# Kernel tuning notes

Hardware: AMD Instinct MI355X
Metric: run time of the kernel (lower is better)

Reference implementation:

```python
import jax, jax.numpy as jnp
import numpy as np

N = 100000      # entities
E = 400000      # triples (KG1)
EH = 400000     # half of symmetric all-edge list
R = 2000        # relations (rel1_size)
RH = 100        # r_hidden
EHID = 300      # e_hidden
LGE = 60000     # line-graph edges
NEG_SLOPE = 0.01


def seg_softmax(e, idx, num):
    # PyG-style segment softmax with max-subtraction and +1e-16 denom
    m = jax.ops.segment_max(e, idx, num_segments=num)
    p = jnp.exp(e - m[idx])
    s = jax.ops.segment_sum(p, idx, num_segments=num)
    return p / (s[idx] + 1e-16)


def gcn(x, w, ei):
    j, i = ei[0], ei[1]
    deg = jax.ops.segment_sum(jnp.ones(ei.shape[1], x.dtype), i, num_segments=x.shape[0])
    dinv = jnp.where(deg > 0, deg ** -0.5, 0.0)
    norm = dinv[j] * dinv[i]                       # [E]
    xw = x @ w.T                                   # [N,300]
    out = jax.ops.segment_sum(norm[:, None] * xw[j], i, num_segments=x.shape[0])
    return jax.nn.relu(out)


def highway(x1, x2, w, b):
    g = jax.nn.sigmoid(x1 @ w.T + b)
    return g * x2 + (1.0 - g) * x1


def l_gat(x, ei, val):
    j, i = ei[0], ei[1]
    n = x.shape[0]
    vi = seg_softmax(val, i, n)
    vj = seg_softmax(val, j, n)
    alpha = seg_softmax(vi + vj, j, n)
    return jax.nn.relu(jax.ops.segment_sum(alpha[:, None] * x[j], i, num_segments=n))


def gat(x, r_emb, ei, rel_e, a_i, a_j, a_r):
    j, i = ei[0], ei[1]
    e = (x @ a_i)[i] + (x @ a_j)[j] + (r_emb @ a_r)[rel_e]
    alpha = seg_softmax(jax.nn.leaky_relu(e, NEG_SLOPE), i, x.shape[0])
    return jax.nn.relu(jax.ops.segment_sum(alpha[:, None] * x[j], i, num_segments=x.shape[0]))


def gat_r_to_e(x_e, x_r, ei, rel_e, a_h, a_t, a_r):
    h, t = ei[0], ei[1]
    n_e = x_e.shape[0]
    eh = (x_e @ a_h)[h]
    et = (x_e @ a_t)[t]
    er = (x_r @ a_r)[rel_e]
    a1 = seg_softmax(jax.nn.leaky_relu(eh + er, NEG_SLOPE), h, n_e)
    x_h = jax.ops.segment_sum(a1[:, None] * x_r[rel_e], h, num_segments=n_e)
    a2 = seg_softmax(jax.nn.leaky_relu(et + er, NEG_SLOPE), t, n_e)
    x_t = jax.ops.segment_sum(a2[:, None] * x_r[rel_e], t, num_segments=n_e)
    return jnp.concatenate([x_h, x_t], axis=1)


def setup_inputs() -> dict:
    key = jax.random.key(0)
    ks = jax.random.split(key, 24)
    # symmetric all-edge graph (guarantees nonzero degrees at touched nodes)
    src = jax.random.randint(ks[0], (EH,), 0, N, dtype=jnp.int32)
    dst = jax.random.randint(ks[1], (EH,), 0, N, dtype=jnp.int32)
    edge_index_all = jnp.stack([jnp.concatenate([src, dst]), jnp.concatenate([dst, src])])
    rel_all = jax.random.randint(ks[2], (2 * EH,), 0, 2 * R, dtype=jnp.int32)
    edge_index = jnp.stack([jax.random.randint(ks[3], (E,), 0, N, dtype=jnp.int32),
                            jax.random.randint(ks[4], (E,), 0, N, dtype=jnp.int32)])
    rel = jax.random.randint(ks[5], (E,), 0, R, dtype=jnp.int32)
    lg_merge = jax.random.randint(ks[6], (2, LGE), 0, R, dtype=jnp.int32)
    lg_triangular = jax.random.randint(ks[7], (2, LGE), 0, R, dtype=jnp.int32)
    merge_val = jax.random.normal(ks[8], (LGE,), jnp.float32)
    tri_val = jax.random.normal(ks[9], (LGE,), jnp.float32)
    x_e = jax.random.normal(ks[10], (N, EHID), jnp.float32)
    s = 0.05
    return {
        'x_e': x_e, 'merge_val': merge_val, 'tri_val': tri_val,
        'gcn1_w': s * jax.random.normal(ks[11], (EHID, EHID), jnp.float32),
        'hw1_w': s * jax.random.normal(ks[12], (EHID, EHID), jnp.float32),
        'hw1_b': jnp.zeros((EHID,), jnp.float32),
        'gcn2_w': s * jax.random.normal(ks[13], (EHID, EHID), jnp.float32),
        'hw2_w': s * jax.random.normal(ks[14], (EHID, EHID), jnp.float32),
        'hw2_b': jnp.zeros((EHID,), jnp.float32),
        'rel_emb_out1': s * jax.random.normal(ks[15], (R, RH), jnp.float32),
        'rel_emb_tri1': s * jax.random.normal(ks[16], (R, RH), jnp.float32),
        'hwr_w': s * jax.random.normal(ks[17], (RH, RH), jnp.float32),
        'hwr_b': jnp.zeros((RH,), jnp.float32),
        'gat_ai': s * jax.random.normal(ks[18], (EHID,), jnp.float32),
        'gat_aj': s * jax.random.normal(ks[19], (EHID,), jnp.float32),
        'gat_ar': s * jax.random.normal(ks[20], (2 * RH,), jnp.float32),
        'g2e_ah': s * jax.random.normal(ks[21], (2 * EHID,), jnp.float32),
        'g2e_at': s * jax.random.normal(ks[22], (2 * EHID,), jnp.float32),
        'g2e_ar': s * jax.random.normal(ks[23], (RH,), jnp.float32),
        'edge_index': edge_index, 'rel': rel,
        'edge_index_all': edge_index_all, 'rel_all': rel_all,
        'lg_merge': lg_merge, 'lg_triangular': lg_triangular,
    }


def reference(x_e, merge_val, tri_val, gcn1_w, hw1_w, hw1_b, gcn2_w, hw2_w, hw2_b,
              rel_emb_out1, rel_emb_tri1, hwr_w, hwr_b, gat_ai, gat_aj, gat_ar,
              g2e_ah, g2e_at, g2e_ar, edge_index, rel, edge_index_all, rel_all,
              lg_merge, lg_triangular):
    x = highway(x_e, gcn(x_e, gcn1_w, edge_index_all), hw1_w, hw1_b)
    x = highway(x, gcn(x, gcn2_w, edge_index_all), hw2_w, hw2_b)
    # rel.max()+1 == rel1_size branch (KG1)
    rel_merge = l_gat(rel_emb_out1, lg_merge, merge_val)      # [R,RH]
    rel_tri = l_gat(rel_emb_tri1, lg_triangular, tri_val)     # [R,RH]
    x_r = highway(rel_merge, rel_tri, hwr_w, hwr_b)           # [R,RH]
    rel_cat = jnp.concatenate([rel_merge, rel_tri], axis=1)   # [R,2RH]
    rel_emb = jnp.concatenate([rel_cat, rel_cat], axis=0)     # [2R,2RH]
    x = jnp.concatenate([x, gat(x, rel_emb, edge_index_all, rel_all, gat_ai, gat_aj, gat_ar)], axis=1)  # [N,600]
    x = jnp.concatenate([x, gat_r_to_e(x, x_r, edge_index, rel, g2e_ah, g2e_at, g2e_ar)], axis=1)        # [N,800]
    return x
```

## Files before the change

kernel.cpp:

```cpp
#include <hip/hip_runtime.h>

#define WAVE 64
#define CDIV(a,b) (((a)+(b)-1)/(b))
#define XBS 320

typedef float f32x16 __attribute__((ext_vector_type(16)));
typedef unsigned short u16x8 __attribute__((ext_vector_type(8)));

__device__ __forceinline__ unsigned short f2bf_rne(float f) {
    unsigned u = __float_as_uint(f);
    unsigned r = (u + 0x7FFFu + ((u >> 16) & 1u)) >> 16;
    return (unsigned short)r;
}
__device__ __forceinline__ float bf2f(unsigned short h) {
    return __uint_as_float(((unsigned)h) << 16);
}
__device__ __forceinline__ float2 bfp2f(ushort2 u) {
    float2 r; r.x = bf2f(u.x); r.y = bf2f(u.y); return r;
}
__device__ __forceinline__ float sigm(float x) { return 1.0f / (1.0f + expf(-x)); }

#define MFMA32(acc, a, b) \
    asm volatile("v_mfma_f32_32x32x16_bf16 %0, %1, %2, %0" : "+v"(acc) : "v"(a), "v"(b))

__device__ __forceinline__ unsigned f2mono(float f) {
    unsigned u = __float_as_uint(f);
    return (u & 0x80000000u) ? ~u : (u | 0x80000000u);
}
__device__ __forceinline__ float mono2f(unsigned u) {
    return (u & 0x80000000u) ? __uint_as_float(u & 0x7fffffffu) : __uint_as_float(~u);
}
__device__ __forceinline__ float leaky(float v) { return (v > 0.0f) ? v : 0.01f*v; }

__device__ __forceinline__ long fragoff(long r, int k, int npk) {
    return ((r >> 5) * (long)npk + (k >> 4)) * 512
         + (((k >> 3) & 1) << 8) + ((r & 31) << 3) + (k & 7);
}

__global__ void k_cvt_pack1(const float* __restrict__ src, long ld, int rows, int K, int npk,
                            int roff, unsigned short* __restrict__ dst)
{
    int nc4 = npk << 2;
    long idx = (long)blockIdx.x*blockDim.x + threadIdx.x;
    if (idx >= (long)rows * nc4) return;
    long r = idx / nc4; int k = (int)(idx % nc4) << 2;
    float4 v = {0.0f, 0.0f, 0.0f, 0.0f};
    if (k + 4 <= K) v = *(const float4*)(src + r*ld + k);
    ushort4 h;
    h.x = f2bf_rne(v.x); h.y = f2bf_rne(v.y); h.z = f2bf_rne(v.z); h.w = f2bf_rne(v.w);
    *(ushort4*)(dst + fragoff(r + roff, k, npk)) = h;
}

__global__ void k_cvt_w4(const float* __restrict__ g1w, const float* __restrict__ h1w,
                         const float* __restrict__ g2w, const float* __restrict__ h2w,
                         int npk, unsigned short* __restrict__ W0,
                         unsigned short* __restrict__ W1)
{
    const int nc4 = npk << 2;
    const long per = (long)300 * nc4;
    long idx = (long)blockIdx.x*blockDim.x + threadIdx.x;
    if (idx >= 4*per) return;
    int which = (int)(idx / per);
    long lidx = idx % per;
    long r = lidx / nc4; int k = (int)(lidx % nc4) << 2;
    const float* src = (which == 0) ? g1w : (which == 1) ? h1w : (which == 2) ? g2w : h2w;
    unsigned short* dst = (which < 2) ? W0 : W1;
    int roff = (which & 1) ? 320 : 0;
    float4 v = {0.0f, 0.0f, 0.0f, 0.0f};
    if (k + 4 <= 300) v = *(const float4*)(src + r*300 + k);
    ushort4 h;
    h.x = f2bf_rne(v.x); h.y = f2bf_rne(v.y); h.z = f2bf_rne(v.z); h.w = f2bf_rne(v.w);
    *(ushort4*)(dst + fragoff(r + roff, k, npk)) = h;
}

__global__ __launch_bounds__(256, 3)
void k_gemm_frag(const unsigned short* __restrict__ Ab,
                 const unsigned short* __restrict__ Bb,
                 unsigned short* __restrict__ C, long ldc, int M, int N, int nk, int nrb)
{
    const int lane = threadIdx.x & 63;
    const int wid  = threadIdx.x >> 6;
    const int lin  = blockIdx.x;
    const int xcd  = lin & 7;
    const int m    = lin >> 3;
    const int col0 = (m % 5) * 128;
    const int rb   = xcd + ((m / 5) << 3);
    if (rb >= nrb) return;
    const int row0 = rb * 128 + wid * 32;

    const long cs = (long)nk * 512;
    const unsigned short* pA = Ab + (long)(row0 >> 5) * cs + lane * 8;
    const unsigned short* pB = Bb + (long)(col0 >> 5) * cs + lane * 8;

    f32x16 acc[4];
    #pragma unroll
    for (int c = 0; c < 4; ++c) acc[c] = (f32x16)0.0f;

    u16x8 pa, pb0, pb1, pb2, pb3;
    u16x8 qa, qb0, qb1, qb2, qb3;

    #define LOADP(t_) { long o = (long)(t_)*512;                                   \
        pa  = *(const u16x8*)(pA + o);                                             \
        pb0 = *(const u16x8*)(pB + o);        pb1 = *(const u16x8*)(pB + cs + o);  \
        pb2 = *(const u16x8*)(pB + 2*cs + o); pb3 = *(const u16x8*)(pB + 3*cs + o); }
    #define LOADQ(t_) { long o = (long)(t_)*512;                                   \
        qa  = *(const u16x8*)(pA + o);                                             \
        qb0 = *(const u16x8*)(pB + o);        qb1 = *(const u16x8*)(pB + cs + o);  \
        qb2 = *(const u16x8*)(pB + 2*cs + o); qb3 = *(const u16x8*)(pB + 3*cs + o); }
    #define STEPP {                                                                 \
        MFMA32(acc[0], pa, pb0); MFMA32(acc[1], pa, pb1);                           \
        MFMA32(acc[2], pa, pb2); MFMA32(acc[3], pa, pb3); }
    #define STEPQ {                                                                 \
        MFMA32(acc[0], qa, qb0); MFMA32(acc[1], qa, qb1);                           \
        MFMA32(acc[2], qa, qb2); MFMA32(acc[3], qa, qb3); }

    LOADP(0);
    int t = 0;
    for (;;) {
        bool m1 = (t + 1 < nk);
        if (m1) LOADQ(t + 1);
        STEPP;
        if (!m1) break;
        bool m2 = (t + 2 < nk);
        if (m2) LOADP(t + 2);
        STEPQ;
        if (!m2) break;
        t += 2;
    }
    #undef LOADP
    #undef LOADQ
    #undef STEPP
    #undef STEPQ

    const int crow0 = row0 + 4*(lane >> 5);
    const int ccol0 = col0 + (lane & 31);
    #pragma unroll
    for (int c = 0; c < 4; ++c) {
        int col = ccol0 + c*32;
        if (col >= N) continue;
        #pragma unroll
        for (int reg = 0; reg < 16; ++reg) {
            int row = crow0 + (reg & 3) + 8*(reg >> 2);
            if (row < M) C[(long)row*ldc + col] = f2bf_rne(acc[c][reg]);
        }
    }
}

#define GBM 64
#define GBN 64
#define GBK 16
__global__ __launch_bounds__(256)
void k_gemm(const float* __restrict__ A, long lda,
            const float* __restrict__ B, long ldb,
            float* __restrict__ C, long ldc,
            int M, int N, int K)
{
    __shared__ float As[GBK][GBM + 4];
    __shared__ float Bs[GBK][GBN + 4];
    const int tid = threadIdx.x;
    const int tx = tid & 15, ty = tid >> 4;
    const int row0 = blockIdx.y * GBM, col0 = blockIdx.x * GBN;
    float acc[4][4] = {};
    for (int kt = 0; kt < K; kt += GBK) {
        #pragma unroll
        for (int p = 0; p < 4; ++p) {
            int mn = (tid >> 4) + p * 16;
            int k  = tid & 15;
            int gk = kt + k;
            int gr = row0 + mn;
            As[k][mn] = (gr < M && gk < K) ? A[(long)gr * lda + gk] : 0.0f;
            int gc = col0 + mn;
            Bs[k][mn] = (gc < N && gk < K) ? B[(long)gc * ldb + gk] : 0.0f;
        }
        __syncthreads();
        #pragma unroll
        for (int kk = 0; kk < GBK; ++kk) {
            float a0 = As[kk][ty*4+0], a1 = As[kk][ty*4+1];
            float a2 = As[kk][ty*4+2], a3 = As[kk][ty*4+3];
            float b0 = Bs[kk][tx*4+0], b1 = Bs[kk][tx*4+1];
            float b2 = Bs[kk][tx*4+2], b3 = Bs[kk][tx*4+3];
            acc[0][0] += a0*b0; acc[0][1] += a0*b1; acc[0][2] += a0*b2; acc[0][3] += a0*b3;
            acc[1][0] += a1*b0; acc[1][1] += a1*b1; acc[1][2] += a1*b2; acc[1][3] += a1*b3;
            acc[2][0] += a2*b0; acc[2][1] += a2*b1; acc[2][2] += a2*b2; acc[2][3] += a2*b3;
            acc[3][0] += a3*b0; acc[3][1] += a3*b1; acc[3][2] += a3*b2; acc[3][3] += a3*b3;
        }
        __syncthreads();
    }
    #pragma unroll
    for (int i2 = 0; i2 < 4; ++i2)
        #pragma unroll
        for (int j2 = 0; j2 < 4; ++j2) {
            int r = row0 + ty*4 + i2, c = col0 + tx*4 + j2;
            if (r < M && c < N) C[(long)r*ldc + c] = acc[i2][j2];
        }
}

__global__ void k_hist3(const int* __restrict__ iA, const int* __restrict__ hE,
                        const int* __restrict__ tE, int* __restrict__ cnt,
                        int EA, int E, int N) {
    int e = blockIdx.x*blockDim.x + threadIdx.x;
    int tot = EA + 2*E;
    if (e >= tot) return;
    if (e < EA)            atomicAdd(&cnt[iA[e]], 1);
    else if (e < EA + E)   atomicAdd(&cnt[N + hE[e - EA]], 1);
    else                   atomicAdd(&cnt[2*N + tE[e - EA - E]], 1);
}
__global__ void k_scan1(const int* __restrict__ in, int* __restrict__ out,
                        int* __restrict__ bsum, int n) {
    __shared__ int sh[512];
    int gid = blockIdx.x*512 + threadIdx.x;
    int v = (gid < n) ? in[gid] : 0;
    sh[threadIdx.x] = v; __syncthreads();
    for (int o = 1; o < 512; o <<= 1) {
        int t = (threadIdx.x >= o) ? sh[threadIdx.x - o] : 0;
        __syncthreads();
        sh[threadIdx.x] += t;
        __syncthreads();
    }
    if (gid < n) out[gid] = sh[threadIdx.x] - v;
    if (threadIdx.x == 511) bsum[blockIdx.x] = sh[511];
}
__global__ void k_scan2(int* __restrict__ bsum, int nb) {
    __shared__ int sh[1024];
    int v = (threadIdx.x < nb) ? bsum[threadIdx.x] : 0;
    sh[threadIdx.x] = v; __syncthreads();
    for (int o = 1; o < 1024; o <<= 1) {
        int t = (threadIdx.x >= o) ? sh[threadIdx.x - o] : 0;
        __syncthreads();
        sh[threadIdx.x] += t;
        __syncthreads();
    }
    if (threadIdx.x < nb) bsum[threadIdx.x] = sh[threadIdx.x] - v;
}
__global__ void k_scan3(int* __restrict__ out, const int* __restrict__ bsum, int n) {
    int gid = blockIdx.x*512 + threadIdx.x;
    if (gid < n) out[gid] += bsum[blockIdx.x];
}
__global__ void k_fill3(const int* __restrict__ iA, const int* __restrict__ hE,
                        const int* __restrict__ tE, const int* __restrict__ rowptr,
                        int* __restrict__ cursor, int* __restrict__ perm,
                        int EA, int E, int N) {
    int e = blockIdx.x*blockDim.x + threadIdx.x;
    int tot = EA + 2*E;
    if (e >= tot) return;
    int key, le;
    if (e < EA)          { le = e;          key = iA[le]; }
    else if (e < EA + E) { le = e - EA;     key = N + hE[le]; }
    else                 { le = e - EA - E; key = 2*N + tE[le]; }
    int p = rowptr[key] + atomicAdd(&cursor[key], 1);
    perm[p] = le;
}
__global__ void k_dinv_cnt(const int* __restrict__ cnt, float* __restrict__ dinv, int n) {
    int i = blockIdx.x*blockDim.x + threadIdx.x;
    if (i < n) { int c = cnt[i]; dinv[i] = (c > 0) ? rsqrtf((float)c) : 0.0f; }
}
__global__ void k_prep_gcn(const int* __restrict__ perm, const int* __restrict__ jA,
                           const int* __restrict__ iA, const float* __restrict__ dinv,
                           int* __restrict__ jp, float* __restrict__ nm, int E) {
    int p = blockIdx.x*blockDim.x + threadIdx.x;
    if (p >= E) return;
    int e = perm[p];
    int j = jA[e];
    jp[p] = j;
    nm[p] = dinv[iA[e]] * dinv[j];
}
__global__ void k_permute3(const int* __restrict__ rel_all, const int* __restrict__ rel,
                           const int* __restrict__ perm, int* __restrict__ relp,
                           int EA, int E, int R) {
    int p = blockIdx.x*blockDim.x + threadIdx.x;
    int tot = EA + 2*E;
    if (p >= tot) return;
    if (p < EA) relp[p] = rel_all[perm[p]] % R;
    else        relp[p] = rel[perm[p]];
}

__global__ void k_gather_hw(const unsigned short* __restrict__ xg, long ldx,
                            const unsigned short* __restrict__ gl,
                            const float* __restrict__ x1f,
                            const unsigned short* __restrict__ x1b,
                            const float* __restrict__ bias,
                            const int* __restrict__ jp, const float* __restrict__ nm,
                            const int* __restrict__ rowptr, const int* __restrict__ cnt,
                            float* __restrict__ outp, long ldo,
                            unsigned short* __restrict__ pk,
                            unsigned short* __restrict__ xbf,
                            const float* __restrict__ ai, const float* __restrict__ aj,
                            float* __restrict__ sa, float* __restrict__ sb,
                            int npk, int n)
{
    int w = (blockIdx.x*blockDim.x + threadIdx.x) >> 6;
    int lane = threadIdx.x & 63;
    if (w >= n) return;
    int beg = rowptr[w], end = beg + cnt[w];
    const int i0 = lane, i1 = lane + 64, i2 = lane + 128;
    const bool t3 = (lane < 22);
    float2 a0 = {0,0}, a1 = {0,0}, a2 = {0,0};
    int e = beg;
    for (; e + 8 <= end; e += 8) {
        long jj[8]; float wt[8];
        #pragma unroll
        for (int u = 0; u < 8; ++u) { jj[u] = jp[e+u]; wt[u] = nm[e+u]; }
        #pragma unroll
        for (int u = 0; u < 8; ++u) {
            float2 v = bfp2f(((const ushort2*)(xg + jj[u]*ldx))[i0]);
            a0.x += wt[u]*v.x; a0.y += wt[u]*v.y;
        }
        #pragma unroll
        for (int u = 0; u < 8; ++u) {
            float2 v = bfp2f(((const ushort2*)(xg + jj[u]*ldx))[i1]);
            a1.x += wt[u]*v.x; a1.y += wt[u]*v.y;
        }
        if (t3) {
            #pragma unroll
            for (int u = 0; u < 8; ++u) {
                float2 v = bfp2f(((const ushort2*)(xg + jj[u]*ldx))[i2]);
                a2.x += wt[u]*v.x; a2.y += wt[u]*v.y;
            }
        }
    }
    for (; e + 4 <= end; e += 4) {
        long jj[4]; float wt[4];
        #pragma unroll
        for (int u = 0; u < 4; ++u) { jj[u] = jp[e+u]; wt[u] = nm[e+u]; }
        #pragma unroll
        for (int u = 0; u < 4; ++u) {
            float2 v = bfp2f(((const ushort2*)(xg + jj[u]*ldx))[i0]);
            a0.x += wt[u]*v.x; a0.y += wt[u]*v.y;
        }
        #pragma unroll
        for (int u = 0; u < 4; ++u) {
            float2 v = bfp2f(((const ushort2*)(xg + jj[u]*ldx))[i1]);
            a1.x += wt[u]*v.x; a1.y += wt[u]*v.y;
        }
        if (t3) {
            #pragma unroll
            for (int u = 0; u < 4; ++u) {
                float2 v = bfp2f(((const ushort2*)(xg + jj[u]*ldx))[i2]);
                a2.x += wt[u]*v.x; a2.y += wt[u]*v.y;
            }
        }
    }
    for (; e < end; ++e) {
        long j0 = jp[e]; float w0 = nm[e];
        float2 v;
        v = bfp2f(((const ushort2*)(xg + j0*ldx))[i0]); a0.x += w0*v.x; a0.y += w0*v.y;
        v = bfp2f(((const ushort2*)(xg + j0*ldx))[i1]); a1.x += w0*v.x; a1.y += w0*v.y;
        if (t3) { v = bfp2f(((const ushort2*)(xg + j0*ldx))[i2]); a2.x += w0*v.x; a2.y += w0*v.y; }
    }
    const ushort2* glr = (const ushort2*)(gl + (long)w*ldx);
    const float2*  x1r = (const float2*)(x1f + (long)w*300);
    const ushort2* x1r2 = (const ushort2*)(x1b + (long)w*XBS);
    const float2*  br  = (const float2*)bias;
    float2 o0 = {0,0}, o1 = {0,0}, o2 = {0,0};
    {
        float2 gv = bfp2f(glr[i0]); float2 bv = br[i0];
        float2 xv = x1f ? x1r[i0] : bfp2f(x1r2[i0]);
        float g0 = sigm(gv.x + bv.x), g1 = sigm(gv.y + bv.y);
        o0.x = g0*fmaxf(a0.x,0.0f) + (1.0f-g0)*xv.x;
        o0.y = g1*fmaxf(a0.y,0.0f) + (1.0f-g1)*xv.y;
    }
    {
        float2 gv = bfp2f(glr[i1]); float2 bv = br[i1];
        float2 xv = x1f ? x1r[i1] : bfp2f(x1r2[i1]);
        float g0 = sigm(gv.x + bv.x), g1 = sigm(gv.y + bv.y);
        o1.x = g0*fmaxf(a1.x,0.0f) + (1.0f-g0)*xv.x;
        o1.y = g1*fmaxf(a1.y,0.0f) + (1.0f-g1)*xv.y;
    }
    if (t3) {
        float2 gv = bfp2f(glr[i2]); float2 bv = br[i2];
        float2 xv = x1f ? x1r[i2] : bfp2f(x1r2[i2]);
        float g0 = sigm(gv.x + bv.x), g1 = sigm(gv.y + bv.y);
        o2.x = g0*fmaxf(a2.x,0.0f) + (1.0f-g0)*xv.x;
        o2.y = g1*fmaxf(a2.y,0.0f) + (1.0f-g1)*xv.y;
    }
    if (outp) {
        float2* dst = (float2*)(outp + (long)w*ldo);
        dst[i0] = o0; dst[i1] = o1;
        if (t3) dst[i2] = o2;
    }
    if (pk) {
        auto pack2 = [&](int k, float2 o) {
            ushort2 hv; hv.x = f2bf_rne(o.x); hv.y = f2bf_rne(o.y);
            *(ushort2*)(pk + fragoff(w, k, npk)) = hv;
        };
        pack2(2*lane, o0);
        pack2(128 + 2*lane, o1);
        if (t3) pack2(256 + 2*lane, o2);
        else if (lane < 24) {
            ushort2 z = {0,0};
            *(ushort2*)(pk + fragoff(w, 256 + 2*lane, npk)) = z;
        }
    }
    if (xbf) {
        ushort2* xw = (ushort2*)(xbf + (long)w*XBS);
        ushort2 t;
        t.x = f2bf_rne(o0.x); t.y = f2bf_rne(o0.y); xw[i0] = t;
        t.x = f2bf_rne(o1.x); t.y = f2bf_rne(o1.y); xw[i1] = t;
        if (t3) { t.x = f2bf_rne(o2.x); t.y = f2bf_rne(o2.y); xw[i2] = t; }
    }
    if (sa) {
        const float2* ai2 = (const float2*)ai;
        const float2* aj2 = (const float2*)aj;
        float2 A0 = ai2[i0], A1 = ai2[i1], J0 = aj2[i0], J1 = aj2[i1];
        float sva = o0.x*A0.x + o0.y*A0.y + o1.x*A1.x + o1.y*A1.y;
        float svb = o0.x*J0.x + o0.y*J0.y + o1.x*J1.x + o1.y*J1.y;
        if (t3) {
            float2 A2 = ai2[i2], J2 = aj2[i2];
            sva += o2.x*A2.x + o2.y*A2.y;
            svb += o2.x*J2.x + o2.y*J2.y;
        }
        #pragma unroll
        for (int o = 32; o > 0; o >>= 1) {
            sva += __shfl_down(sva, o);
            svb += __shfl_down(svb, o);
        }
        if (lane == 0) { sa[w] = sva; sb[w] = svb; }
    }
}

__global__ void k_gat300(const unsigned short* __restrict__ xbf,
                         const float* __restrict__ sA, const float* __restrict__ sB,
                         const float* __restrict__ rsc,
                         const int* __restrict__ jp, const int* __restrict__ relp,
                         const int* __restrict__ rowptr, const int* __restrict__ cnt,
                         float* __restrict__ out, long ldo,
                         const float* __restrict__ ah, const float* __restrict__ at,
                         float* __restrict__ sh, float* __restrict__ st,
                         int n)
{
    int w = (blockIdx.x*blockDim.x + threadIdx.x) >> 6;
    int lane = threadIdx.x & 63;
    if (w >= n) return;
    int beg = rowptr[w], c = cnt[w];
    const int i0 = lane, i1 = lane + 64, i2 = lane + 128;
    const bool t3 = (lane < 22);
    float2 a0 = {0,0}, a1 = {0,0}, a2 = {0,0};
    if (c > 0) {
        float base = sA[w];
        int   jc = 0;
        float sval = -3.4e38f;
        if (lane < c) {
            jc = jp[beg + lane];
            sval = leaky(base + sB[jc] + rsc[relp[beg + lane]]);
        }
        float mx = sval;
        for (int t = 64 + lane; t < c; t += 64)
            mx = fmaxf(mx, leaky(base + sB[jp[beg+t]] + rsc[relp[beg+t]]));
        #pragma unroll
        for (int o = 32; o > 0; o >>= 1) mx = fmaxf(mx, __shfl_xor(mx, o));
        float pexp = (lane < c) ? expf(sval - mx) : 0.0f;
        float ss = pexp;
        for (int t = 64 + lane; t < c; t += 64)
            ss += expf(leaky(base + sB[jp[beg+t]] + rsc[relp[beg+t]]) - mx);
        #pragma unroll
        for (int o = 32; o > 0; o >>= 1) ss += __shfl_xor(ss, o);
        float inv = 1.0f / (ss + 1e-16f);
        int q = 0;
        int cc = (c < 64) ? c : 64;
        for (; q + 8 <= cc; q += 8) {
            float al[8]; long jj[8];
            #pragma unroll
            for (int u = 0; u < 8; ++u) {
                al[u] = __shfl(pexp, q+u) * inv;
                jj[u] = __shfl(jc, q+u);
            }
            #pragma unroll
            for (int u = 0; u < 8; ++u) {
                float2 v = bfp2f(((const ushort2*)(xbf + jj[u]*XBS))[i0]);
                a0.x += al[u]*v.x; a0.y += al[u]*v.y;
            }
            #pragma unroll
            for (int u = 0; u < 8; ++u) {
                float2 v = bfp2f(((const ushort2*)(xbf + jj[u]*XBS))[i1]);
                a1.x += al[u]*v.x; a1.y += al[u]*v.y;
            }
            if (t3) {
                #pragma unroll
                for (int u = 0; u < 8; ++u) {
                    float2 v = bfp2f(((const ushort2*)(xbf + jj[u]*XBS))[i2]);
                    a2.x += al[u]*v.x; a2.y += al[u]*v.y;
                }
            }
        }
        for (; q + 4 <= cc; q += 4) {
            float al[4]; long jj[4];
            #pragma unroll
            for (int u = 0; u < 4; ++u) {
                al[u] = __shfl(pexp, q+u) * inv;
                jj[u] = __shfl(jc, q+u);
            }
            #pragma unroll
            for (int u = 0; u < 4; ++u) {
                float2 v = bfp2f(((const ushort2*)(xbf + jj[u]*XBS))[i0]);
                a0.x += al[u]*v.x; a0.y += al[u]*v.y;
            }
            #pragma unroll
            for (int u = 0; u < 4; ++u) {
                float2 v = bfp2f(((const ushort2*)(xbf + jj[u]*XBS))[i1]);
                a1.x += al[u]*v.x; a1.y += al[u]*v.y;
            }
            if (t3) {
                #pragma unroll
                for (int u = 0; u < 4; ++u) {
                    float2 v = bfp2f(((const ushort2*)(xbf + jj[u]*XBS))[i2]);
                    a2.x += al[u]*v.x; a2.y += al[u]*v.y;
                }
            }
        }
        for (; q < c; ++q) {
            float al; long j0;
            if (q < 64) { al = __shfl(pexp, q) * inv; j0 = __shfl(jc, q); }
            else {
                j0 = jp[beg + q];
                al = expf(leaky(base + sB[(int)j0] + rsc[relp[beg+q]]) - mx) * inv;
            }
            float2 v;
            v = bfp2f(((const ushort2*)(xbf + j0*XBS))[i0]); a0.x += al*v.x; a0.y += al*v.y;
            v = bfp2f(((const ushort2*)(xbf + j0*XBS))[i1]); a1.x += al*v.x; a1.y += al*v.y;
            if (t3) { v = bfp2f(((const ushort2*)(xbf + j0*XBS))[i2]); a2.x += al*v.x; a2.y += al*v.y; }
        }
    }
    a0.x = fmaxf(a0.x, 0.0f); a0.y = fmaxf(a0.y, 0.0f);
    a1.x = fmaxf(a1.x, 0.0f); a1.y = fmaxf(a1.y, 0.0f);
    a2.x = fmaxf(a2.x, 0.0f); a2.y = fmaxf(a2.y, 0.0f);
    float2* dst = (float2*)(out + (long)w*ldo);
    dst[i0] = a0; dst[i1] = a1;
    if (t3) dst[i2] = a2;
    {
        const ushort2* xw = (const ushort2*)(xbf + (long)w*XBS);
        const float2* ahL = (const float2*)ah;
        const float2* atL = (const float2*)at;
        const float2* ahH = (const float2*)(ah + 300);
        const float2* atH = (const float2*)(at + 300);
        float2 x0 = bfp2f(xw[i0]), x1v = bfp2f(xw[i1]);
        float svh = x0.x*ahL[i0].x + x0.y*ahL[i0].y + x1v.x*ahL[i1].x + x1v.y*ahL[i1].y
                  + a0.x*ahH[i0].x + a0.y*ahH[i0].y + a1.x*ahH[i1].x + a1.y*ahH[i1].y;
        float svt = x0.x*atL[i0].x + x0.y*atL[i0].y + x1v.x*atL[i1].x + x1v.y*atL[i1].y
                  + a0.x*atH[i0].x + a0.y*atH[i0].y + a1.x*atH[i1].x + a1.y*atH[i1].y;
        if (t3) {
            float2 x2v = bfp2f(xw[i2]);
            svh += x2v.x*ahL[i2].x + x2v.y*ahL[i2].y + a2.x*ahH[i2].x + a2.y*ahH[i2].y;
            svt += x2v.x*atL[i2].x + x2v.y*atL[i2].y + a2.x*atH[i2].x + a2.y*atH[i2].y;
        }
        #pragma unroll
        for (int o = 32; o > 0; o >>= 1) {
            svh += __shfl_down(svh, o);
            svt += __shfl_down(svt, o);
        }
        if (lane == 0) { sh[w] = svh; st[w] = svt; }
    }
}

__global__ void k_gather_rel2(const float* __restrict__ xr,
                              const float* __restrict__ sH, const float* __restrict__ sT,
                              const float* __restrict__ srel,
                              const int* __restrict__ relp,
                              const int* __restrict__ rowptrH, const int* __restrict__ cntH,
                              const int* __restrict__ rowptrT, const int* __restrict__ cntT,
                              float* __restrict__ out, long ldo, int n)
{
    int gw = (blockIdx.x*blockDim.x + threadIdx.x) >> 6;
    int lane = threadIdx.x & 63;
    if (gw >= 2*n) return;
    const bool isT = (gw >= n);
    const int w = isT ? gw - n : gw;
    const float* snode = isT ? sT : sH;
    const int* rowptr = isT ? rowptrT : rowptrH;
    const int* cnt    = isT ? cntT    : cntH;
    float* dst = out + (isT ? 700 : 600) + (long)w*ldo;
    int beg = rowptr[w], c = cnt[w];
    const bool t0 = (lane < 50);
    float2 a0 = {0,0};
    if (c > 0) {
        float base = snode[w];
        int   rc = 0;
        float sval = -3.4e38f;
        if (lane < c) {
            rc = relp[beg + lane];
            sval = leaky(base + srel[rc]);
        }
        float mx = sval;
        for (int t = 64 + lane; t < c; t += 64)
            mx = fmaxf(mx, leaky(base + srel[relp[beg+t]]));
        #pragma unroll
        for (int o = 32; o > 0; o >>= 1) mx = fmaxf(mx, __shfl_xor(mx, o));
        float pexp = (lane < c) ? expf(sval - mx) : 0.0f;
        float ss = pexp;
        for (int t = 64 + lane; t < c; t += 64)
            ss += expf(leaky(base + srel[relp[beg+t]]) - mx);
        #pragma unroll
        for (int o = 32; o > 0; o >>= 1) ss += __shfl_xor(ss, o);
        float inv = 1.0f / (ss + 1e-16f);
        int q = 0;
        int cc = (c < 64) ? c : 64;
        for (; q + 4 <= cc; q += 4) {
            float al0 = __shfl(pexp, q)   * inv;
            float al1 = __shfl(pexp, q+1) * inv;
            float al2 = __shfl(pexp, q+2) * inv;
            float al3 = __shfl(pexp, q+3) * inv;
            long r0i = __shfl(rc, q), r1i = __shfl(rc, q+1);
            long r2i = __shfl(rc, q+2), r3i = __shfl(rc, q+3);
            if (t0) {
                float2 v;
                v = ((const float2*)(xr + r0i*100))[lane]; a0.x += al0*v.x; a0.y += al0*v.y;
                v = ((const float2*)(xr + r1i*100))[lane]; a0.x += al1*v.x; a0.y += al1*v.y;
                v = ((const float2*)(xr + r2i*100))[lane]; a0.x += al2*v.x; a0.y += al2*v.y;
                v = ((const float2*)(xr + r3i*100))[lane]; a0.x += al3*v.x; a0.y += al3*v.y;
            }
        }
        for (; q < c; ++q) {
            float al; long r0i;
            if (q < 64) { al = __shfl(pexp, q) * inv; r0i = __shfl(rc, q); }
            else {
                r0i = relp[beg + q];
                al = expf(leaky(base + srel[(int)r0i]) - mx) * inv;
            }
            if (t0) {
                float2 v = ((const float2*)(xr + r0i*100))[lane];
                a0.x += al*v.x; a0.y += al*v.y;
            }
        }
    }
    if (t0) ((float2*)dst)[lane] = a0;
}

__global__ void k_lgat_max(const float* __restrict__ mval, const float* __restrict__ tval,
                           const int* __restrict__ iM, const int* __restrict__ jM,
                           const int* __restrict__ iT, const int* __restrict__ jT,
                           unsigned* __restrict__ mi, unsigned* __restrict__ mj,
                           int LGE, int R)
{
    int e = blockIdx.x*blockDim.x + threadIdx.x;
    if (e >= 2*LGE) return;
    bool g1 = e >= LGE; int le = g1 ? e - LGE : e;
    float v = g1 ? tval[le] : mval[le];
    int i = (g1 ? iT[le] : iM[le]) + (g1 ? R : 0);
    int j = (g1 ? jT[le] : jM[le]) + (g1 ? R : 0);
    unsigned mv = f2mono(v);
    atomicMax(&mi[i], mv);
    atomicMax(&mj[j], mv);
}
__global__ void k_lgat_sum(const float* __restrict__ mval, const float* __restrict__ tval,
                           const int* __restrict__ iM, const int* __restrict__ jM,
                           const int* __restrict__ iT, const int* __restrict__ jT,
                           const unsigned* __restrict__ mi, const unsigned* __restrict__ mj,
                           float* __restrict__ si, float* __restrict__ sj,
                           int LGE, int R)
{
    int e = blockIdx.x*blockDim.x + threadIdx.x;
    if (e >= 2*LGE) return;
    bool g1 = e >= LGE; int le = g1 ? e - LGE : e;
    float v = g1 ? tval[le] : mval[le];
    int i = (g1 ? iT[le] : iM[le]) + (g1 ? R : 0);
    int j = (g1 ? jT[le] : jM[le]) + (g1 ? R : 0);
    atomicAdd(&si[i], expf(v - mono2f(mi[i])));
    atomicAdd(&sj[j], expf(v - mono2f(mj[j])));
}
__global__ void k_lgat_vsum2(const float* __restrict__ mval, const float* __restrict__ tval,
                             const int* __restrict__ iM, const int* __restrict__ jM,
                             const int* __restrict__ iT, const int* __restrict__ jT,
                             const unsigned* __restrict__ mi, const float* __restrict__ si,
                             const unsigned* __restrict__ mj, const float* __restrict__ sj,
                             float* __restrict__ vsum, int LGE, int R)
{
    int e = blockIdx.x*blockDim.x + threadIdx.x;
    if (e >= 2*LGE) return;
    bool g1 = e >= LGE; int le = g1 ? e - LGE : e;
    float v = g1 ? tval[le] : mval[le];
    int i = (g1 ? iT[le] : iM[le]) + (g1 ? R : 0);
    int j = (g1 ? jT[le] : jM[le]) + (g1 ? R : 0);
    float pi = expf(v - mono2f(mi[i])) / (si[i] + 1e-16f);
    float pj = expf(v - mono2f(mj[j])) / (sj[j] + 1e-16f);
    vsum[e] = pi + pj;
}
__global__ void k_lgat_max2(const float* __restrict__ vsum,
                            const int* __restrict__ jM, const int* __restrict__ jT,
                            unsigned* __restrict__ m2, int LGE, int R)
{
    int e = blockIdx.x*blockDim.x + threadIdx.x;
    if (e >= 2*LGE) return;
    bool g1 = e >= LGE; int le = g1 ? e - LGE : e;
    int j = (g1 ? jT[le] : jM[le]) + (g1 ? R : 0);
    atomicMax(&m2[j], f2mono(vsum[e]));
}
__global__ void k_lgat_sum2(const float* __restrict__ vsum,
                            const int* __restrict__ jM, const int* __restrict__ jT,
                            const unsigned* __restrict__ m2, float* __restrict__ s2,
                            int LGE, int R)
{
    int e = blockIdx.x*blockDim.x + threadIdx.x;
    if (e >= 2*LGE) return;
    bool g1 = e >= LGE; int le = g1 ? e - LGE : e;
    int j = (g1 ? jT[le] : jM[le]) + (g1 ? R : 0);
    atomicAdd(&s2[j], expf(vsum[e] - mono2f(m2[j])));
}
__global__ void k_lgat_agg(const float* __restrict__ vsum,
                           const unsigned* __restrict__ m2, const float* __restrict__ s2,
                           const int* __restrict__ iM, const int* __restrict__ jM,
                           const int* __restrict__ iT, const int* __restrict__ jT,
                           const float* __restrict__ remb1, const float* __restrict__ remb2,
                           float* __restrict__ obuf, int LGE, int R, int RH)
{
    int w = (blockIdx.x*blockDim.x + threadIdx.x) >> 6;
    int lane = threadIdx.x & 63;
    if (w >= 2*LGE) return;
    bool g1 = w >= LGE; int le = g1 ? w - LGE : w;
    int o = g1 ? R : 0;
    int i = (g1 ? iT[le] : iM[le]) + o;
    int j = (g1 ? jT[le] : jM[le]);
    float alpha = expf(vsum[w] - mono2f(m2[o + j])) / (s2[o + j] + 1e-16f);
    const float* x = g1 ? remb2 : remb1;
    const float4* src = (const float4*)(x + (long)j*RH);
    float* dst = obuf + (long)i*RH;
    if (lane < 25) {
        float4 v = src[lane];
        atomicAdd(&dst[lane*4+0], alpha*v.x);
        atomicAdd(&dst[lane*4+1], alpha*v.y);
        atomicAdd(&dst[lane*4+2], alpha*v.z);
        atomicAdd(&dst[lane*4+3], alpha*v.w);
    }
}
__global__ void k_relu2d(float* __restrict__ p, long rows, int cols, long ld) {
    long idx = (long)blockIdx.x*blockDim.x + threadIdx.x;
    if (idx >= rows*(long)cols) return;
    long r = idx / cols; int c = (int)(idx % cols);
    float v = p[r*ld+c];
    p[r*ld+c] = fmaxf(v, 0.0f);
}

__global__ void k_highway(const float* __restrict__ x1, long ld1,
                          const float* __restrict__ gl, long ldg,
                          const float* __restrict__ x2, long ld2,
                          const float* __restrict__ bias,
                          float* __restrict__ out, long ldo,
                          long rows, int F, int relu_x2)
{
    long idx = (long)blockIdx.x*blockDim.x + threadIdx.x;
    if (idx >= rows * (long)F) return;
    long r = idx / F; int c = (int)(idx % F);
    float g = 1.0f / (1.0f + expf(-(gl[r*ldg+c] + bias[c])));
    float v2 = x2[r*ld2+c]; if (relu_x2) v2 = fmaxf(v2, 0.0f);
    float v1 = x1[r*ld1+c];
    out[r*ldo+c] = g*v2 + (1.0f-g)*v1;
}

__global__ void k_rowdot2(const float* __restrict__ x, long ldx, int rows, int K,
                          const float* __restrict__ a, const float* __restrict__ b,
                          float* __restrict__ oa, float* __restrict__ ob)
{
    int w = (blockIdx.x*blockDim.x + threadIdx.x) >> 6;
    int lane = threadIdx.x & 63;
    if (w >= rows) return;
    const float* xr = x + (long)w*ldx;
    float sa = 0.0f, sb = 0.0f;
    for (int k = lane; k < K; k += WAVE) {
        float v = xr[k];
        sa += v * a[k];
        if (b) sb += v * b[k];
    }
    #pragma unroll
    for (int off = 32; off > 0; off >>= 1) {
        sa += __shfl_down(sa, off);
        if (b) sb += __shfl_down(sb, off);
    }
    if (lane == 0) { oa[w] = sa; if (ob) ob[w] = sb; }
}

__global__ void k_relscore(const float* __restrict__ mg, const float* __restrict__ tr,
                           const float* __restrict__ ar, float* __restrict__ out, int R, int RH)
{
    int w = (blockIdx.x*blockDim.x + threadIdx.x) >> 6;
    int lane = threadIdx.x & 63;
    if (w >= R) return;
    float s = 0.0f;
    for (int k = lane; k < RH; k += WAVE)
        s += mg[(long)w*RH+k]*ar[k] + tr[(long)w*RH+k]*ar[RH+k];
    #pragma unroll
    for (int off = 32; off > 0; off >>= 1) s += __shfl_down(s, off);
    if (lane == 0) out[w] = s;
}

extern "C" void kernel_launch(void* const* d_in, const int* in_sizes, int n_in,
                              void* d_out, int out_size, void* d_ws, size_t ws_size,
                              hipStream_t stream)
{
    const float* x_e   = (const float*)d_in[0];
    const float* mval  = (const float*)d_in[1];
    const float* tval  = (const float*)d_in[2];
    const float* g1w   = (const float*)d_in[3];
    const float* h1w   = (const float*)d_in[4];
    const float* h1b   = (const float*)d_in[5];
    const float* g2w   = (const float*)d_in[6];
    const float* h2w   = (const float*)d_in[7];
    const float* h2b   = (const float*)d_in[8];
    const float* remb1 = (const float*)d_in[9];
    const float* remb2 = (const float*)d_in[10];
    const float* hrw   = (const float*)d_in[11];
    const float* hrb   = (const float*)d_in[12];
    const float* gat_ai= (const float*)d_in[13];
    const float* gat_aj= (const float*)d_in[14];
    const float* gat_ar= (const float*)d_in[15];
    const float* g2e_ah= (const float*)d_in[16];
    const float* g2e_at= (const float*)d_in[17];
    const float* g2e_ar= (const float*)d_in[18];
    const int* edge_index     = (const int*)d_in[19];
    const int* rel            = (const int*)d_in[20];
    const int* edge_index_all = (const int*)d_in[21];
    const int* rel_all        = (const int*)d_in[22];
    const int* lg_merge       = (const int*)d_in[23];
    const int* lg_tri         = (const int*)d_in[24];

    const int F    = 300;
    const int RH   = 100;
    const int Kp   = 304;
    const int npk  = Kp / 16;
    const int N    = in_sizes[0] / F;
    const int E    = in_sizes[20];
    const int EA   = in_sizes[22];
    const int LGE  = in_sizes[1];
    const int R    = in_sizes[9] / RH;
    const long OUTC = 800;
    const int Mpad = CDIV(N, 128) * 128;
    const int NB   = 640;
    const long LDC = 640;

    const int* jA = edge_index_all;
    const int* iA = edge_index_all + EA;
    const int* hE = edge_index;
    const int* tE = edge_index + E;
    const int* jM = lg_merge;  const int* iM = lg_merge + LGE;
    const int* jT = lg_tri;    const int* iT = lg_tri  + LGE;

    float* ws = (float*)d_ws;
    size_t off = 0;
    auto alloc = [&](size_t n) { float* p = ws + off; off += (n + 15) & ~(size_t)15; return p; };
    unsigned short* Ascr = (unsigned short*)alloc((size_t)N*NB/2);
    unsigned short* Axb = (unsigned short*)alloc((size_t)Mpad*Kp/2);
    unsigned short* xbf = (unsigned short*)alloc((size_t)N*XBS/2);
    unsigned short* Wb  = (unsigned short*)alloc((size_t)2*NB*Kp/2);
    unsigned short* W0 = Wb;
    unsigned short* W1 = Wb + (size_t)NB*Kp;
    float*    dinv = alloc(N);
    float*    sA_  = alloc(N);
    float*    sB_  = alloc(N);
    float*    sH_  = alloc(N);
    float*    sT_  = alloc(N);
    float*    xr   = alloc((size_t)R*RH);
    float*    xrg  = alloc((size_t)R*RH);
    float*    lg   = alloc((size_t)12*R + (size_t)2*R*RH);
    unsigned* lmi  = (unsigned*)lg;          float* lsi = lg + 2*R;
    unsigned* lmj  = (unsigned*)(lg + 4*R);  float* lsj = lg + 6*R;
    unsigned* lm2  = (unsigned*)(lg + 8*R);  float* ls2 = lg + 10*R;
    float*    obuf = lg + 12*R;
    float*    mrg  = obuf;
    float*    tri  = obuf + (size_t)R*RH;
    float*    vsum = alloc((size_t)2*LGE);
    float*    rsc  = alloc(R);
    float*    srel = alloc(R);
    int*   bsum    = (int*)alloc(1024);
    int*   cntAll  = (int*)alloc((size_t)6*N);
    int*   curAll  = cntAll + 3*N;
    int*   rowptrG = (int*)alloc((size_t)3*N);
    int*   permAll = (int*)alloc((size_t)EA + 2*E);
    int*   relpAll = (int*)alloc((size_t)EA + 2*E);
    int*   jpA     = (int*)alloc(EA);
    float* nmA     = alloc(EA);

    float* out = (float*)d_out;

    const int  nrb = CDIV(N, 128);
    const int  gemmBlocks = 8 * CDIV(nrb, 8) * 5;
    const int  gatherGrid = CDIV(N, 4);
    const int  cvtBigGrid = CDIV((long)N * (Kp/4), 256);
    const int  cvtW4Grid  = CDIV((long)4 * 300 * (Kp/4), 256);
    const int  ETOT = EA + 2*E;
    const int  nb3 = CDIV(3*N, 512);

    hipMemsetAsync(Wb, 0, (size_t)2*NB*Kp*2, stream);
    hipMemsetAsync(Axb + (size_t)N*Kp, 0, (size_t)(Mpad-N)*Kp*2, stream);
    k_cvt_w4<<<cvtW4Grid,256,0,stream>>>(g1w, h1w, g2w, h2w, npk, W0, W1);
    k_cvt_pack1<<<cvtBigGrid,256,0,stream>>>(x_e, 300, N, 300, npk, 0, Axb);

    hipMemsetAsync(cntAll, 0, (size_t)6*N*4, stream);
    k_hist3<<<CDIV(ETOT,256),256,0,stream>>>(iA, hE, tE, cntAll, EA, E, N);
    k_scan1<<<nb3,512,0,stream>>>(cntAll, rowptrG, bsum, 3*N);
    k_scan2<<<1,1024,0,stream>>>(bsum, nb3);
    k_scan3<<<nb3,512,0,stream>>>(rowptrG, bsum, 3*N);
    k_fill3<<<CDIV(ETOT,256),256,0,stream>>>(iA, hE, tE, rowptrG, curAll, permAll, EA, E, N);
    k_dinv_cnt<<<CDIV(N,256),256,0,stream>>>(cntAll, dinv, N);
    k_prep_gcn<<<CDIV(EA,256),256,0,stream>>>(permAll, jA, iA, dinv, jpA, nmA, EA);
    k_permute3<<<CDIV(ETOT,256),256,0,stream>>>(rel_all, rel, permAll, relpAll, EA, E, R);

    k_gemm_frag<<<gemmBlocks,256,0,stream>>>(Axb, W0, Ascr, LDC, N, 620, npk, nrb);
    k_gather_hw<<<gatherGrid,256,0,stream>>>(Ascr, LDC, Ascr+320,
                                             x_e, (const unsigned short*)nullptr, h1b,
                                             jpA, nmA, rowptrG, cntAll,
                                             (float*)nullptr, OUTC, Axb, xbf,
                                             (const float*)nullptr, (const float*)nullptr,
                                             (float*)nullptr, (float*)nullptr, npk, N);

    k_gemm_frag<<<gemmBlocks,256,0,stream>>>(Axb, W1, Ascr, LDC, N, 620, npk, nrb);
    k_gather_hw<<<gatherGrid,256,0,stream>>>(Ascr, LDC, Ascr+320,
                                             (const float*)nullptr, xbf, h2b,
                                             jpA, nmA, rowptrG, cntAll,
                                             out, OUTC, (unsigned short*)nullptr, xbf,
                                             gat_ai, gat_aj, sA_, sB_, npk, N);

    hipMemsetAsync(lg, 0, ((size_t)12*R + (size_t)2*R*RH)*4, stream);
    const int lgGrid = CDIV(2*LGE, 256);
    k_lgat_max  <<<lgGrid,256,0,stream>>>(mval, tval, iM, jM, iT, jT, lmi, lmj, LGE, R);
    k_lgat_sum  <<<lgGrid,256,0,stream>>>(mval, tval, iM, jM, iT, jT, lmi, lmj, lsi, lsj, LGE, R);
    k_lgat_vsum2<<<lgGrid,256,0,stream>>>(mval, tval, iM, jM, iT, jT, lmi, lsi, lmj, lsj,
                                          vsum, LGE, R);
    k_lgat_max2 <<<lgGrid,256,0,stream>>>(vsum, jM, jT, lm2, LGE, R);
    k_lgat_sum2 <<<lgGrid,256,0,stream>>>(vsum, jM, jT, lm2, ls2, LGE, R);
    k_lgat_agg  <<<CDIV(2*LGE*64,256),256,0,stream>>>(vsum, lm2, ls2, iM, jM, iT, jT,
                                                      remb1, remb2, obuf, LGE, R, RH);
    k_relu2d    <<<CDIV((long)2*R*RH,256),256,0,stream>>>(obuf, 2*R, RH, RH);

    dim3 gridR(CDIV(RH,GBN), CDIV(R,GBM));
    k_gemm<<<gridR,256,0,stream>>>(mrg, RH, hrw, RH, xrg, RH, R, RH, RH);
    k_highway<<<CDIV((long)R*RH,256),256,0,stream>>>(mrg, RH, xrg, RH, tri, RH, hrb, xr, RH, R, RH, 0);

    k_relscore<<<CDIV((long)R*64,256),256,0,stream>>>(mrg, tri, gat_ar, rsc, R, RH);

    k_gat300<<<gatherGrid,256,0,stream>>>(xbf, sA_, sB_, rsc, jpA, relpAll,
                                          rowptrG, cntAll, out+300, OUTC,
                                          g2e_ah, g2e_at, sH_, sT_, N);

    k_rowdot2<<<CDIV((long)R*64,256),256,0,stream>>>(xr, RH, R, RH, g2e_ar, (const float*)nullptr,
                                                     srel, (float*)nullptr);
    k_gather_rel2<<<CDIV(2*N,4),256,0,stream>>>(xr, sH_, sT_, srel, relpAll,
                                                rowptrG + N, cntAll + N,
                                                rowptrG + 2*N, cntAll + 2*N,
                                                out, OUTC, N);
}
```

Baseline: 1.223 ms.

## Fuse CSR fill with edge prep and store relation embeddings as bf16

Merges the CSR fill, degree-normalisation, GCN edge prep and relation permute kernels into one pass that writes jp, nm and relp directly, dropping the perm array and its extra gather passes. The two relation-score kernels are merged into one launch, which also writes a bf16 copy of x_r padded to 128 columns. The relation gather kernel then reads that half-width copy. This cuts launches and memory traffic but lowers the precision of the gathered relation features to bf16, and the edge-to-slot assignment still depends on atomic order.

```diff
diff --git a/kernel.cpp b/kernel.cpp
--- a/kernel.cpp
+++ b/kernel.cpp
@@ -236,42 +236,39 @@
     int gid = blockIdx.x*512 + threadIdx.x;
     if (gid < n) out[gid] += bsum[blockIdx.x];
 }
-__global__ void k_fill3(const int* __restrict__ iA, const int* __restrict__ hE,
-                        const int* __restrict__ tE, const int* __restrict__ rowptr,
-                        int* __restrict__ cursor, int* __restrict__ perm,
-                        int EA, int E, int N) {
+__global__ void k_fill3f(const int* __restrict__ iA, const int* __restrict__ jA,
+                         const int* __restrict__ hE, const int* __restrict__ tE,
+                         const int* __restrict__ rel_all, const int* __restrict__ rel,
+                         const int* __restrict__ rowptr, const int* __restrict__ cnt,
+                         int* __restrict__ cursor,
+                         int* __restrict__ jp, float* __restrict__ nm,
+                         int* __restrict__ relp,
+                         int EA, int E, int N, int R) {
     int e = blockIdx.x*blockDim.x + threadIdx.x;
     int tot = EA + 2*E;
     if (e >= tot) return;
-    int key, le;
-    if (e < EA)          { le = e;          key = iA[le]; }
-    else if (e < EA + E) { le = e - EA;     key = N + hE[le]; }
-    else                 { le = e - EA - E; key = 2*N + tE[le]; }
-    int p = rowptr[key] + atomicAdd(&cursor[key], 1);
-    perm[p] = le;
-}
-__global__ void k_dinv_cnt(const int* __restrict__ cnt, float* __restrict__ dinv, int n) {
-    int i = blockIdx.x*blockDim.x + threadIdx.x;
-    if (i < n) { int c = cnt[i]; dinv[i] = (c > 0) ? rsqrtf((float)c) : 0.0f; }
-}
-__global__ void k_prep_gcn(const int* __restrict__ perm, const int* __restrict__ jA,
-                           const int* __restrict__ iA, const float* __restrict__ dinv,
-                           int* __restrict__ jp, float* __restrict__ nm, int E) {
-    int p = blockIdx.x*blockDim.x + threadIdx.x;
-    if (p >= E) return;
-    int e = perm[p];
-    int j = jA[e];
-    jp[p] = j;
-    nm[p] = dinv[iA[e]] * dinv[j];
-}
-__global__ void k_permute3(const int* __restrict__ rel_all, const int* __restrict__ rel,
-                           const int* __restrict__ perm, int* __restrict__ relp,
-                           int EA, int E, int R) {
-    int p = blockIdx.x*blockDim.x + threadIdx.x;
-    int tot = EA + 2*E;
-    if (p >= tot) return;
-    if (p < EA) relp[p] = rel_all[perm[p]] % R;
-    else        relp[p] = rel[perm[p]];
+    if (e < EA) {
+        int le = e;
+        int i = iA[le];
+        int p = rowptr[i] + atomicAdd(&cursor[i], 1);
+        int j = jA[le];
+        jp[p] = j;
+        float di = rsqrtf((float)cnt[i]);
+        int cj = cnt[j];
+        float dj = (cj > 0) ? rsqrtf((float)cj) : 0.0f;
+        nm[p] = di * dj;
+        relp[p] = rel_all[le] % R;
+    } else if (e < EA + E) {
+        int le = e - EA;
+        int key = N + hE[le];
+        int p = rowptr[key] + atomicAdd(&cursor[key], 1);
+        relp[p] = rel[le];
+    } else {
+        int le = e - EA - E;
+        int key = 2*N + tE[le];
+        int p = rowptr[key] + atomicAdd(&cursor[key], 1);
+        relp[p] = rel[le];
+    }
 }
 
 __global__ void k_gather_hw(const unsigned short* __restrict__ xg, long ldx,
@@ -551,7 +548,7 @@
     }
 }
 
-__global__ void k_gather_rel2(const float* __restrict__ xr,
+__global__ void k_gather_rel2(const unsigned short* __restrict__ xrb,
                               const float* __restrict__ sH, const float* __restrict__ sT,
                               const float* __restrict__ srel,
                               const int* __restrict__ relp,
@@ -602,10 +599,10 @@
             long r2i = __shfl(rc, q+2), r3i = __shfl(rc, q+3);
             if (t0) {
                 float2 v;
-                v = ((const float2*)(xr + r0i*100))[lane]; a0.x += al0*v.x; a0.y += al0*v.y;
-                v = ((const float2*)(xr + r1i*100))[lane]; a0.x += al1*v.x; a0.y += al1*v.y;
-                v = ((const float2*)(xr + r2i*100))[lane]; a0.x += al2*v.x; a0.y += al2*v.y;
-                v = ((const float2*)(xr + r3i*100))[lane]; a0.x += al3*v.x; a0.y += al3*v.y;
+                v = bfp2f(((const ushort2*)(xrb + r0i*128))[lane]); a0.x += al0*v.x; a0.y += al0*v.y;
+                v = bfp2f(((const ushort2*)(xrb + r1i*128))[lane]); a0.x += al1*v.x; a0.y += al1*v.y;
+                v = bfp2f(((const ushort2*)(xrb + r2i*128))[lane]); a0.x += al2*v.x; a0.y += al2*v.y;
+                v = bfp2f(((const ushort2*)(xrb + r3i*128))[lane]); a0.x += al3*v.x; a0.y += al3*v.y;
             }
         }
         for (; q < c; ++q) {
@@ -616,7 +613,7 @@
                 al = expf(leaky(base + srel[(int)r0i]) - mx) * inv;
             }
             if (t0) {
-                float2 v = ((const float2*)(xr + r0i*100))[lane];
+                float2 v = bfp2f(((const ushort2*)(xrb + r0i*128))[lane]);
                 a0.x += al*v.x; a0.y += al*v.y;
             }
         }
@@ -744,40 +741,37 @@
     out[r*ldo+c] = g*v2 + (1.0f-g)*v1;
 }
 
-__global__ void k_rowdot2(const float* __restrict__ x, long ldx, int rows, int K,
-                          const float* __restrict__ a, const float* __restrict__ b,
-                          float* __restrict__ oa, float* __restrict__ ob)
-{
-    int w = (blockIdx.x*blockDim.x + threadIdx.x) >> 6;
+__global__ void k_rs2(const float* __restrict__ mg, const float* __restrict__ tr,
+                      const float* __restrict__ ar,
+                      const float* __restrict__ xr, const float* __restrict__ g2e_ar,
+                      float* __restrict__ rsc, float* __restrict__ srel,
+                      unsigned short* __restrict__ xrb, int R, int RH)
+{
+    int gw = (blockIdx.x*blockDim.x + threadIdx.x) >> 6;
     int lane = threadIdx.x & 63;
-    if (w >= rows) return;
-    const float* xr = x + (long)w*ldx;
-    float sa = 0.0f, sb = 0.0f;
-    for (int k = lane; k < K; k += WAVE) {
-        float v = xr[k];
-        sa += v * a[k];
-        if (b) sb += v * b[k];
-    }
-    #pragma unroll
-    for (int off = 32; off > 0; off >>= 1) {
-        sa += __shfl_down(sa, off);
-        if (b) sb += __shfl_down(sb, off);
-    }
-    if (lane == 0) { oa[w] = sa; if (ob) ob[w] = sb; }
-}
-
-__global__ void k_relscore(const float* __restrict__ mg, const float* __restrict__ tr,
-                           const float* __restrict__ ar, float* __restrict__ out, int R, int RH)
-{
-    int w = (blockIdx.x*blockDim.x + threadIdx.x) >> 6;
-    int lane = threadIdx.x & 63;
-    if (w >= R) return;
+    if (gw >= 2*R) return;
     float s = 0.0f;
-    for (int k = lane; k < RH; k += WAVE)
-        s += mg[(long)w*RH+k]*ar[k] + tr[(long)w*RH+k]*ar[RH+k];
-    #pragma unroll
-    for (int off = 32; off > 0; off >>= 1) s += __shfl_down(s, off);
-    if (lane == 0) out[w] = s;
+    if (gw < R) {
+        for (int k = lane; k < RH; k += WAVE)
+            s += mg[(long)gw*RH+k]*ar[k] + tr[(long)gw*RH+k]*ar[RH+k];
+        #pragma unroll
+        for (int off = 32; off > 0; off >>= 1) s += __shfl_down(s, off);
+        if (lane == 0) rsc[gw] = s;
+    } else {
+        int r = gw - R;
+        #pragma unroll
+        for (int t = 0; t < 2; ++t) {
+            int k = lane + t*64;
+            if (k < RH) {
+                float v = xr[(long)r*RH + k];
+                s += v * g2e_ar[k];
+                xrb[(long)r*128 + k] = f2bf_rne(v);
+            }
+        }
+        #pragma unroll
+        for (int off = 32; off > 0; off >>= 1) s += __shfl_down(s, off);
+        if (lane == 0) srel[r] = s;
+    }
 }
 
 extern "C" void kernel_launch(void* const* d_in, const int* in_sizes, int n_in,
@@ -840,7 +834,7 @@
     unsigned short* Wb  = (unsigned short*)alloc((size_t)2*NB*Kp/2);
     unsigned short* W0 = Wb;
     unsigned short* W1 = Wb + (size_t)NB*Kp;
-    float*    dinv = alloc(N);
+    unsigned short* xrb = (unsigned short*)alloc((size_t)R*128/2);
     float*    sA_  = alloc(N);
     float*    sB_  = alloc(N);
     float*    sH_  = alloc(N);
@@ -861,7 +855,6 @@
     int*   cntAll  = (int*)alloc((size_t)6*N);
     int*   curAll  = cntAll + 3*N;
     int*   rowptrG = (int*)alloc((size_t)3*N);
-    int*   permAll = (int*)alloc((size_t)EA + 2*E);
     int*   relpAll = (int*)alloc((size_t)EA + 2*E);
     int*   jpA     = (int*)alloc(EA);
     float* nmA     = alloc(EA);
@@ -886,10 +879,9 @@
     k_scan1<<<nb3,512,0,stream>>>(cntAll, rowptrG, bsum, 3*N);
     k_scan2<<<1,1024,0,stream>>>(bsum, nb3);
     k_scan3<<<nb3,512,0,stream>>>(rowptrG, bsum, 3*N);
-    k_fill3<<<CDIV(ETOT,256),256,0,stream>>>(iA, hE, tE, rowptrG, curAll, permAll, EA, E, N);
-    k_dinv_cnt<<<CDIV(N,256),256,0,stream>>>(cntAll, dinv, N);
-    k_prep_gcn<<<CDIV(EA,256),256,0,stream>>>(permAll, jA, iA, dinv, jpA, nmA, EA);
-    k_permute3<<<CDIV(ETOT,256),256,0,stream>>>(rel_all, rel, permAll, relpAll, EA, E, R);
+    k_fill3f<<<CDIV(ETOT,256),256,0,stream>>>(iA, jA, hE, tE, rel_all, rel,
+                                              rowptrG, cntAll, curAll,
+                                              jpA, nmA, relpAll, EA, E, N, R);
 
     k_gemm_frag<<<gemmBlocks,256,0,stream>>>(Axb, W0, Ascr, LDC, N, 620, npk, nrb);
     k_gather_hw<<<gatherGrid,256,0,stream>>>(Ascr, LDC, Ascr+320,
@@ -922,15 +914,14 @@
     k_gemm<<<gridR,256,0,stream>>>(mrg, RH, hrw, RH, xrg, RH, R, RH, RH);
     k_highway<<<CDIV((long)R*RH,256),256,0,stream>>>(mrg, RH, xrg, RH, tri, RH, hrb, xr, RH, R, RH, 0);
 
-    k_relscore<<<CDIV((long)R*64,256),256,0,stream>>>(mrg, tri, gat_ar, rsc, R, RH);
+    k_rs2<<<CDIV((long)2*R*64,256),256,0,stream>>>(mrg, tri, gat_ar, xr, g2e_ar,
+                                                   rsc, srel, xrb, R, RH);
 
     k_gat300<<<gatherGrid,256,0,stream>>>(xbf, sA_, sB_, rsc, jpA, relpAll,
                                           rowptrG, cntAll, out+300, OUTC,
                                           g2e_ah, g2e_at, sH_, sT_, N);
 
-    k_rowdot2<<<CDIV((long)R*64,256),256,0,stream>>>(xr, RH, R, RH, g2e_ar, (const float*)nullptr,
-                                                     srel, (float*)nullptr);
-    k_gather_rel2<<<CDIV(2*N,4),256,0,stream>>>(xr, sH_, sT_, srel, relpAll,
+    k_gather_rel2<<<CDIV(2*N,4),256,0,stream>>>(xrb, sH_, sT_, srel, relpAll,
                                                 rowptrG + N, cntAll + N,
                                                 rowptrG + 2*N, cntAll + 2*N,
                                                 out, OUTC, N);
```

Result: no change. 1.206 ms (-1.4%).
